# Optimization experiments

Hardware: AMD Instinct MI355X
Metric: run time of the kernel (lower is better)

## Reference

```python
import jax, jax.numpy as jnp
import numpy as np

N_SEG = 128  # number of distinct batch ids (patients/samples)
N = 250000   # total cells
E = 128      # embed_dim
H = 4        # num_heads

def setup_inputs() -> dict:
    key = jax.random.key(0)
    k1, k2, k3 = jax.random.split(key, 3)
    x = jax.random.normal(k1, (N, E), dtype=jnp.float32)
    weights = jax.random.normal(k2, (H, E), dtype=jnp.float32) * 0.02
    batch = jnp.sort(jax.random.randint(k3, (N,), 0, N_SEG, dtype=jnp.int64))
    return {"x": x, "weights": weights, "batch": batch}

def reference(x, weights, batch):
    # att[n,h] = <x[n], weights[h]>
    att = x @ weights.T  # [N, H]
    # segment-wise (per batch id) stable softmax over the sample axis
    m = jax.lax.stop_gradient(jax.ops.segment_max(att, batch, num_segments=N_SEG))  # [N_SEG, H]
    e = jnp.exp(att - m[batch])                                                     # [N, H]
    s = jax.ops.segment_sum(e, batch, num_segments=N_SEG)                           # [N_SEG, H]
    att_sm = e / s[batch]                                                           # [N, H]
    # h[b, h, e] = sum_{n in segment b} att_sm[n, h] * x[n, e]
    h = jax.ops.segment_sum(att_sm[:, :, None] * x[:, None, :], batch, num_segments=N_SEG)  # [N_SEG, H, E]
    # cat=False -> average over heads
    return h.mean(axis=1)  # [N_SEG, E]
```

## Files before the change

### kernel.cpp

```cpp
#include <hip/hip_runtime.h>

#define EDIM 128
#define NHEAD 4
#define NSEG 128
#define LOG2E 1.4426950408889634f

typedef float f32x8 __attribute__((ext_vector_type(8)));


#define DOT8(xv, wv)                                                     \
    fmaf((xv)[7], (wv)[7], fmaf((xv)[6], (wv)[6],                        \
    fmaf((xv)[5], (wv)[5], fmaf((xv)[4], (wv)[4],                        \
    fmaf((xv)[3], (wv)[3], fmaf((xv)[2], (wv)[2],                        \
    fmaf((xv)[1], (wv)[1], (xv)[0] * (wv)[0])))))))

#define RED16(v) do { v += __shfl_xor(v, 1, 64); v += __shfl_xor(v, 2, 64); \
                      v += __shfl_xor(v, 4, 64); v += __shfl_xor(v, 8, 64); } while (0)
#define REDG(v)  do { v += __shfl_xor(v, 16, 64); v += __shfl_xor(v, 32, 64); } while (0)

#define FLUSH_SEG(seg) do {                                              \
    float t0 = s0, t1 = s1, t2 = s2, t3 = s3;                            \
    REDG(t0); REDG(t1); REDG(t2); REDG(t3);                              \
    if (lane == 0) {                                                     \
        atomicAdd(&s_sum[(seg) * NHEAD + 0], t0);                        \
        atomicAdd(&s_sum[(seg) * NHEAD + 1], t1);                        \
        atomicAdd(&s_sum[(seg) * NHEAD + 2], t2);                        \
        atomicAdd(&s_sum[(seg) * NHEAD + 3], t3);                        \
    }                                                                    \
    f32x8 r0 = a0, r1 = a1, r2 = a2, r3 = a3;                            \
    _Pragma("unroll")                                                    \
    for (int j = 0; j < 8; ++j) {                                        \
        float u0 = r0[j]; REDG(u0); r0[j] = u0;                          \
        float u1 = r1[j]; REDG(u1); r1[j] = u1;                          \
        float u2 = r2[j]; REDG(u2); r2[j] = u2;                          \
        float u3 = r3[j]; REDG(u3); r3[j] = u3;                          \
    }                                                                    \
    f32x8 rv = (g == 0) ? r0 : ((g == 1) ? r1 : ((g == 2) ? r2 : r3));   \
    float* op_ = &outh[((seg) * NHEAD + g) * EDIM + 8 * c];              \
    _Pragma("unroll")                                                    \
    for (int j = 0; j < 8; ++j) atomicAdd(op_ + j, rv[j]);               \
    a0 = Z8; a1 = Z8; a2 = Z8; a3 = Z8;                                  \
    s0 = 0.f; s1 = 0.f; s2 = 0.f; s3 = 0.f;                              \
} while (0)

__global__ __launch_bounds__(256, 1) void attn_agg_pass1(
    const float* __restrict__ x, const float* __restrict__ w,
    const int* __restrict__ batch,
    float* __restrict__ s_sum,
    float* __restrict__ outh,
    int n, int qpw)
{
    const int tid  = blockIdx.x * blockDim.x + threadIdx.x;
    const int wave = tid >> 6;
    const int lane = threadIdx.x & 63;
    const int g    = lane >> 4;
    const int c    = lane & 15;

    const int nquads = (n + 3) >> 2;
    const int q0 = wave * qpw;
    if (q0 >= nquads) return;
    const int q1 = min(q0 + qpw, nquads);

    const float* wp = w + 8 * c;
    const f32x8 w0 = *reinterpret_cast<const f32x8*>(wp + 0 * EDIM);
    const f32x8 w1 = *reinterpret_cast<const f32x8*>(wp + 1 * EDIM);
    const f32x8 w2 = *reinterpret_cast<const f32x8*>(wp + 2 * EDIM);
    const f32x8 w3 = *reinterpret_cast<const f32x8*>(wp + 3 * EDIM);

    const f32x8 Z8 = {0.f, 0.f, 0.f, 0.f, 0.f, 0.f, 0.f, 0.f};
    f32x8 a0 = Z8, a1 = Z8, a2 = Z8, a3 = Z8;
    float s0 = 0.f, s1 = 0.f, s2 = 0.f, s3 = 0.f;

    int cur_b = __builtin_amdgcn_readfirstlane(batch[q0 * 4]);

    for (int q = q0; q < q1; ++q) {
        const int cell = q * 4 + g;
        const int row  = min(cell, n - 1);
        const f32x8 xv = *reinterpret_cast<const f32x8*>(
            x + (size_t)row * EDIM + 8 * c);

        float p0 = DOT8(xv, w0);
        float p1 = DOT8(xv, w1);
        float p2 = DOT8(xv, w2);
        float p3 = DOT8(xv, w3);
        RED16(p0); RED16(p1); RED16(p2); RED16(p3);

        const float e0 = __builtin_exp2f(p0 * LOG2E);
        const float e1 = __builtin_exp2f(p1 * LOG2E);
        const float e2 = __builtin_exp2f(p2 * LOG2E);
        const float e3 = __builtin_exp2f(p3 * LOG2E);

        const bool full = (q * 4 + 3 < n);
        const int  b3   = __builtin_amdgcn_readfirstlane(batch[min(q * 4 + 3, n - 1)]);

        if (full && b3 == cur_b) {
            s0 += e0; s1 += e1; s2 += e2; s3 += e3;
            a0 += xv * e0; a1 += xv * e1; a2 += xv * e2; a3 += xv * e3;
        } else {
            FLUSH_SEG(cur_b);
            if (cell < n) {
                const int my_b = batch[cell];
                if (c == 0) {
                    atomicAdd(&s_sum[my_b * NHEAD + 0], e0);
                    atomicAdd(&s_sum[my_b * NHEAD + 1], e1);
                    atomicAdd(&s_sum[my_b * NHEAD + 2], e2);
                    atomicAdd(&s_sum[my_b * NHEAD + 3], e3);
                }
                float* bp = &outh[(size_t)(my_b * NHEAD) * EDIM + 8 * c];
                f32x8 v;
                v = xv * e0;
#pragma unroll
                for (int j = 0; j < 8; ++j) atomicAdd(bp + 0 * EDIM + j, v[j]);
                v = xv * e1;
#pragma unroll
                for (int j = 0; j < 8; ++j) atomicAdd(bp + 1 * EDIM + j, v[j]);
                v = xv * e2;
#pragma unroll
                for (int j = 0; j < 8; ++j) atomicAdd(bp + 2 * EDIM + j, v[j]);
                v = xv * e3;
#pragma unroll
                for (int j = 0; j < 8; ++j) atomicAdd(bp + 3 * EDIM + j, v[j]);
            }
            cur_b = b3;
        }
    }

    FLUSH_SEG(cur_b);
}

__global__ __launch_bounds__(256) void attn_agg_finish(
    const float* __restrict__ s_sum, const float* __restrict__ outh,
    float* __restrict__ out)
{
    int i = blockIdx.x * blockDim.x + threadIdx.x;
    if (i >= NSEG * EDIM) return;
    int b = i >> 7;
    int d = i & (EDIM - 1);
    float r = 0.f;
#pragma unroll
    for (int h = 0; h < NHEAD; ++h) {
        float s = s_sum[b * NHEAD + h];
        float v = outh[(b * NHEAD + h) * EDIM + d];
        r += (s > 0.f) ? (v / s) : 0.f;
    }
    out[i] = 0.25f * r;
}

extern "C" void kernel_launch(void* const* d_in, const int* in_sizes, int n_in,
                              void* d_out, int out_size, void* d_ws, size_t ws_size,
                              hipStream_t stream) {
    const float* x     = (const float*)d_in[0];
    const float* w     = (const float*)d_in[1];
    const int*   batch = (const int*)d_in[2];
    float* out = (float*)d_out;

    const int n = in_sizes[0] / EDIM;

    float* s_sum = (float*)d_ws;
    float* outh  = s_sum + NSEG * NHEAD;
    const size_t zero_bytes = (size_t)(NSEG * NHEAD + NSEG * NHEAD * EDIM) * sizeof(float);
    hipMemsetAsync(d_ws, 0, zero_bytes, stream);

    const int nquads = (n + 3) >> 2;
    const int qpw    = 16;
    const int nwaves = (nquads + qpw - 1) / qpw;
    const int blocks = (nwaves * 64 + 255) / 256;
    attn_agg_pass1<<<blocks, 256, 0, stream>>>(x, w, batch, s_sum, outh, n, qpw);

    attn_agg_finish<<<(NSEG * EDIM + 255) / 256, 256, 0, stream>>>(s_sum, outh, out);
}
```

Baseline: 251.1 us.

## Replace global atomics with per-wave partial buffers reduced in finish kernel

Each wave now stores up to two per-segment partial results (head-weighted sums and exp sums) into a workspace slot instead of issuing global atomicAdds into a shared per-segment accumulator. Cells at a segment boundary are folded into the flushed or the new accumulator by a mask rather than by per-cell atomics. The finish kernel, one block per segment, scans the segment tags, gathers the matching partials and normalises. This removes the memset and the atomic contention, and relaxes launch bounds to allow more occupancy. In exchange it adds partial writes and reads, and it assumes each wave spans at most two segments.

```diff
diff --git a/kernel.cpp b/kernel.cpp
--- a/kernel.cpp
+++ b/kernel.cpp
@@ -18,15 +18,9 @@
                       v += __shfl_xor(v, 4, 64); v += __shfl_xor(v, 8, 64); } while (0)
 #define REDG(v)  do { v += __shfl_xor(v, 16, 64); v += __shfl_xor(v, 32, 64); } while (0)
 
-#define FLUSH_SEG(seg) do {                                              \
+#define FLUSH_STORE(seg) do {                                            \
     float t0 = s0, t1 = s1, t2 = s2, t3 = s3;                            \
     REDG(t0); REDG(t1); REDG(t2); REDG(t3);                              \
-    if (lane == 0) {                                                     \
-        atomicAdd(&s_sum[(seg) * NHEAD + 0], t0);                        \
-        atomicAdd(&s_sum[(seg) * NHEAD + 1], t1);                        \
-        atomicAdd(&s_sum[(seg) * NHEAD + 2], t2);                        \
-        atomicAdd(&s_sum[(seg) * NHEAD + 3], t3);                        \
-    }                                                                    \
     f32x8 r0 = a0, r1 = a1, r2 = a2, r3 = a3;                            \
     _Pragma("unroll")                                                    \
     for (int j = 0; j < 8; ++j) {                                        \
@@ -36,18 +30,24 @@
         float u3 = r3[j]; REDG(u3); r3[j] = u3;                          \
     }                                                                    \
     f32x8 rv = (g == 0) ? r0 : ((g == 1) ? r1 : ((g == 2) ? r2 : r3));   \
-    float* op_ = &outh[((seg) * NHEAD + g) * EDIM + 8 * c];              \
-    _Pragma("unroll")                                                    \
-    for (int j = 0; j < 8; ++j) atomicAdd(op_ + j, rv[j]);               \
+    const size_t ent_ = (size_t)wave * 2 + (nflushed < 1 ? 0 : 1);       \
+    *reinterpret_cast<f32x8*>(pouth + ent_ * 512 + g * EDIM + 8 * c) = rv; \
+    if (lane == 0) {                                                     \
+        psum[ent_ * 4 + 0] = t0; psum[ent_ * 4 + 1] = t1;                \
+        psum[ent_ * 4 + 2] = t2; psum[ent_ * 4 + 3] = t3;                \
+        pseg[ent_] = (seg);                                              \
+    }                                                                    \
+    nflushed++;                                                          \
     a0 = Z8; a1 = Z8; a2 = Z8; a3 = Z8;                                  \
     s0 = 0.f; s1 = 0.f; s2 = 0.f; s3 = 0.f;                              \
 } while (0)
 
-__global__ __launch_bounds__(256, 1) void attn_agg_pass1(
+__global__ __launch_bounds__(256) void attn_agg_pass1(
     const float* __restrict__ x, const float* __restrict__ w,
     const int* __restrict__ batch,
-    float* __restrict__ s_sum,
-    float* __restrict__ outh,
+    float* __restrict__ pouth,
+    float* __restrict__ psum,
+    int*   __restrict__ pseg,
     int n, int qpw)
 {
     const int tid  = blockIdx.x * blockDim.x + threadIdx.x;
@@ -58,7 +58,10 @@
 
     const int nquads = (n + 3) >> 2;
     const int q0 = wave * qpw;
-    if (q0 >= nquads) return;
+    if (q0 >= nquads) {
+        if (lane == 0) { pseg[(size_t)wave * 2] = -1; pseg[(size_t)wave * 2 + 1] = -1; }
+        return;
+    }
     const int q1 = min(q0 + qpw, nquads);
 
     const float* wp = w + 8 * c;
@@ -70,6 +73,7 @@
     const f32x8 Z8 = {0.f, 0.f, 0.f, 0.f, 0.f, 0.f, 0.f, 0.f};
     f32x8 a0 = Z8, a1 = Z8, a2 = Z8, a3 = Z8;
     float s0 = 0.f, s1 = 0.f, s2 = 0.f, s3 = 0.f;
+    int nflushed = 0;
 
     int cur_b = __builtin_amdgcn_readfirstlane(batch[q0 * 4]);
 
@@ -97,53 +101,62 @@
             s0 += e0; s1 += e1; s2 += e2; s3 += e3;
             a0 += xv * e0; a1 += xv * e1; a2 += xv * e2; a3 += xv * e3;
         } else {
-            FLUSH_SEG(cur_b);
-            if (cell < n) {
-                const int my_b = batch[cell];
-                if (c == 0) {
-                    atomicAdd(&s_sum[my_b * NHEAD + 0], e0);
-                    atomicAdd(&s_sum[my_b * NHEAD + 1], e1);
-                    atomicAdd(&s_sum[my_b * NHEAD + 2], e2);
-                    atomicAdd(&s_sum[my_b * NHEAD + 3], e3);
-                }
-                float* bp = &outh[(size_t)(my_b * NHEAD) * EDIM + 8 * c];
-                f32x8 v;
-                v = xv * e0;
-#pragma unroll
-                for (int j = 0; j < 8; ++j) atomicAdd(bp + 0 * EDIM + j, v[j]);
-                v = xv * e1;
-#pragma unroll
-                for (int j = 0; j < 8; ++j) atomicAdd(bp + 1 * EDIM + j, v[j]);
-                v = xv * e2;
-#pragma unroll
-                for (int j = 0; j < 8; ++j) atomicAdd(bp + 2 * EDIM + j, v[j]);
-                v = xv * e3;
-#pragma unroll
-                for (int j = 0; j < 8; ++j) atomicAdd(bp + 3 * EDIM + j, v[j]);
-            }
+            const int my_b = (cell < n) ? batch[cell] : -2;
+            const bool m1 = (my_b == cur_b);
+            const float f1 = m1 ? 1.f : 0.f;
+            s0 += e0 * f1; s1 += e1 * f1; s2 += e2 * f1; s3 += e3 * f1;
+            a0 += xv * (e0 * f1); a1 += xv * (e1 * f1);
+            a2 += xv * (e2 * f1); a3 += xv * (e3 * f1);
+
+            FLUSH_STORE(cur_b);
             cur_b = b3;
+
+            const float f2 = (!m1 && my_b == cur_b) ? 1.f : 0.f;
+            s0 += e0 * f2; s1 += e1 * f2; s2 += e2 * f2; s3 += e3 * f2;
+            a0 += xv * (e0 * f2); a1 += xv * (e1 * f2);
+            a2 += xv * (e2 * f2); a3 += xv * (e3 * f2);
         }
     }
 
-    FLUSH_SEG(cur_b);
+    FLUSH_STORE(cur_b);
+    if (lane == 0 && nflushed < 2) pseg[(size_t)wave * 2 + 1] = -1;
 }
 
-__global__ __launch_bounds__(256) void attn_agg_finish(
-    const float* __restrict__ s_sum, const float* __restrict__ outh,
-    float* __restrict__ out)
+__global__ __launch_bounds__(512) void attn_agg_finish(
+    const float* __restrict__ pouth, const float* __restrict__ psum,
+    const int* __restrict__ pseg, float* __restrict__ out, int nent)
 {
-    int i = blockIdx.x * blockDim.x + threadIdx.x;
-    if (i >= NSEG * EDIM) return;
-    int b = i >> 7;
-    int d = i & (EDIM - 1);
-    float r = 0.f;
-#pragma unroll
-    for (int h = 0; h < NHEAD; ++h) {
-        float s = s_sum[b * NHEAD + h];
-        float v = outh[(b * NHEAD + h) * EDIM + d];
-        r += (s > 0.f) ? (v / s) : 0.f;
+    const int b = blockIdx.x;
+    const int t = threadIdx.x;
+    const int h = t >> 7, d = t & (EDIM - 1);
+
+    __shared__ int matches[512];
+    __shared__ int nmatch;
+    __shared__ float hacc[NHEAD][EDIM];
+    if (t == 0) nmatch = 0;
+    __syncthreads();
+
+    for (int i = t; i < nent; i += 512) {
+        if (pseg[i] == b) {
+            int p = atomicAdd(&nmatch, 1);
+            matches[p] = i;
+        }
     }
-    out[i] = 0.25f * r;
+    __syncthreads();
+
+    float acc = 0.f, sh = 0.f;
+    const int nm = nmatch;
+    for (int k = 0; k < nm; ++k) {
+        const int i = matches[k];
+        acc += pouth[(size_t)i * 512 + t];
+        sh  += psum[(size_t)i * 4 + h];
+    }
+    hacc[h][d] = (sh > 0.f) ? (acc / sh) : 0.f;
+    __syncthreads();
+
+    if (h == 0)
+        out[b * EDIM + d] = 0.25f *
+            (hacc[0][d] + hacc[1][d] + hacc[2][d] + hacc[3][d]);
 }
 
 extern "C" void kernel_launch(void* const* d_in, const int* in_sizes, int n_in,
@@ -155,17 +168,24 @@
     float* out = (float*)d_out;
 
     const int n = in_sizes[0] / EDIM;
+    const int nquads = (n + 3) >> 2;
 
-    float* s_sum = (float*)d_ws;
-    float* outh  = s_sum + NSEG * NHEAD;
-    const size_t zero_bytes = (size_t)(NSEG * NHEAD + NSEG * NHEAD * EDIM) * sizeof(float);
-    hipMemsetAsync(d_ws, 0, zero_bytes, stream);
+    const size_t per_wave = 2 * (512 * 4 + 4 * 4 + 4);
+    int W = (int)(ws_size / per_wave) - 4;
+    if (W > 4096) W = 4096;
+    if (W < 64)   W = 64;
+    W &= ~3;
 
-    const int nquads = (n + 3) >> 2;
-    const int qpw    = 16;
-    const int nwaves = (nquads + qpw - 1) / qpw;
-    const int blocks = (nwaves * 64 + 255) / 256;
-    attn_agg_pass1<<<blocks, 256, 0, stream>>>(x, w, batch, s_sum, outh, n, qpw);
+    const int qpw      = (nquads + W - 1) / W;
+    const int nw       = (nquads + qpw - 1) / qpw;
+    const int blocks1  = (nw + 3) / 4;
+    const int launched = blocks1 * 4;
+    const int nent     = launched * 2;
 
-    attn_agg_finish<<<(NSEG * EDIM + 255) / 256, 256, 0, stream>>>(s_sum, outh, out);
+    float* pouth = (float*)d_ws;
+    float* psum  = pouth + (size_t)nent * 512;
+    int*   pseg  = (int*)(psum + (size_t)nent * 4);
+
+    attn_agg_pass1<<<blocks1, 256, 0, stream>>>(x, w, batch, pouth, psum, pseg, n, qpw);
+    attn_agg_finish<<<NSEG, 512, 0, stream>>>(pouth, psum, pseg, out, nent);
 }
```

Result: faster. 202.9 us (-19.2%).
